# Optimization experiments

Measured on AMD Instinct MI355X. Metric: run time of the kernel, lower is better.

Reference implementation:

```python
import jax, jax.numpy as jnp
import numpy as np

D_MODEL = 2048
NUM_HEADS = 16
NUM_KV_HEADS = 4
D_HEAD = D_MODEL // NUM_HEADS  # 128
GROUPS = NUM_HEADS // NUM_KV_HEADS  # 4
ROPE_THETA = 10000.0
EPS = 1e-6


def setup_inputs() -> dict:
    key = jax.random.key(0)
    ks = jax.random.split(key, 7)
    B, S = 2, 2048
    s = 1.0 / np.sqrt(D_MODEL)
    return {
        "qkv": jax.random.normal(ks[0], (B, S, D_MODEL), dtype=jnp.float32),
        "Wq": jax.random.normal(ks[1], (D_MODEL, D_MODEL), dtype=jnp.float32) * s,
        "Wk": jax.random.normal(ks[2], (NUM_KV_HEADS * D_HEAD, D_MODEL), dtype=jnp.float32) * s,
        "Wv": jax.random.normal(ks[3], (NUM_KV_HEADS * D_HEAD, D_MODEL), dtype=jnp.float32) * s,
        "Wo": jax.random.normal(ks[4], (D_MODEL, D_MODEL), dtype=jnp.float32) * s,
        "q_gamma": jnp.ones((D_HEAD,), dtype=jnp.float32),
        "k_gamma": jnp.ones((D_HEAD,), dtype=jnp.float32),
    }


def _rmsnorm(x, gamma):
    # per-head RMSNorm over last dim (d_head)
    var = jnp.mean(jnp.square(x), axis=-1, keepdims=True)
    return x * jax.lax.rsqrt(var + EPS) * gamma


def _rope(x, cos, sin):
    # x: [B, S, H, Dh]; cos/sin: [S, Dh]
    half = x.shape[-1] // 2
    x1, x2 = x[..., :half], x[..., half:]
    rot = jnp.concatenate([-x2, x1], axis=-1)
    return x * cos[None, :, None, :] + rot * sin[None, :, None, :]


def reference(qkv, Wq, Wk, Wv, Wo, q_gamma, k_gamma):
    B, S, D = qkv.shape
    q = jnp.einsum("bsd,ed->bse", qkv, Wq).reshape(B, S, NUM_HEADS, D_HEAD)
    k = jnp.einsum("bsd,ed->bse", qkv, Wk).reshape(B, S, NUM_KV_HEADS, D_HEAD)
    v = jnp.einsum("bsd,ed->bse", qkv, Wv).reshape(B, S, NUM_KV_HEADS, D_HEAD)

    q = _rmsnorm(q, q_gamma)
    k = _rmsnorm(k, k_gamma)

    # RoPE, position_ids = arange(S)
    pos = jnp.arange(S, dtype=jnp.float32)
    inv_freq = 1.0 / (ROPE_THETA ** (jnp.arange(0, D_HEAD, 2, dtype=jnp.float32) / D_HEAD))
    ang = pos[:, None] * inv_freq[None, :]                 # [S, Dh/2]
    cos = jnp.concatenate([jnp.cos(ang), jnp.cos(ang)], axis=-1)  # [S, Dh]
    sin = jnp.concatenate([jnp.sin(ang), jnp.sin(ang)], axis=-1)
    q = _rope(q, cos, sin)
    k = _rope(k, cos, sin)

    # [B, H, S, Dh]
    q = q.transpose(0, 2, 1, 3)
    k = k.transpose(0, 2, 1, 3)
    v = v.transpose(0, 2, 1, 3)
    # GQA: repeat kv heads
    k = jnp.repeat(k, GROUPS, axis=1)
    v = jnp.repeat(v, GROUPS, axis=1)

    scale = 1.0 / np.sqrt(D_HEAD)
    scores = jnp.einsum("bhqd,bhkd->bhqk", q, k) * scale
    causal = jnp.tril(jnp.ones((S, S), dtype=bool))
    scores = jnp.where(causal[None, None], scores, jnp.finfo(scores.dtype).min)
    probs = jax.nn.softmax(scores, axis=-1)
    attended = jnp.einsum("bhqk,bhkd->bhqd", probs, v)     # [B, H, S, Dh]
    attended = attended.transpose(0, 2, 1, 3).reshape(B, S, D)
    return jnp.einsum("bsd,ed->bse", attended, Wo)
```

## Files before the change

kernel.cpp:

```cpp
#include <hip/hip_runtime.h>

#define S_LEN 2048
#define B_SZ 2
#define DMODEL 2048
#define NHEADS 16
#define NKV 4
#define DHEAD 128
#define SCALE 0.08838834764831845f
#define KVB 32

typedef __bf16 bf16x8 __attribute__((ext_vector_type(8)));
typedef __bf16 bf16x4 __attribute__((ext_vector_type(4)));
typedef float f32x4 __attribute__((ext_vector_type(4)));

#define MFMA(a, b, c) __builtin_amdgcn_mfma_f32_16x16x32_bf16(a, b, c, 0, 0, 0)

__device__ __forceinline__ void gload_lds16(const __bf16* g, __bf16* l) {
    __builtin_amdgcn_global_load_lds(
        (const __attribute__((address_space(1))) unsigned int*)g,
        (__attribute__((address_space(3))) unsigned int*)l, 16, 0, 0);
}

__global__ __launch_bounds__(256) void convert_kernel(
    const float* __restrict__ s0, const float* __restrict__ s1,
    const float* __restrict__ s2, const float* __restrict__ s3,
    const float* __restrict__ s4,
    __bf16* __restrict__ d0, __bf16* __restrict__ d1, __bf16* __restrict__ d2,
    __bf16* __restrict__ d3, __bf16* __restrict__ d4,
    float* __restrict__ cosT, float* __restrict__ sinT) {
    if (blockIdx.y == 5) {
        int i = blockIdx.x * 256 + threadIdx.x;
        int s = i >> 6, d = i & 63;
        float freq = powf(10000.0f, -(2.0f * (float)d) / 128.0f);
        float ang = (float)s * freq;
        cosT[i] = cosf(ang);
        sinT[i] = sinf(ang);
        return;
    }
    const float* s;
    __bf16* d;
    int n8;
    switch (blockIdx.y) {
        case 0: s = s0; d = d0; n8 = (B_SZ * S_LEN * DMODEL) / 8; break;
        case 1: s = s1; d = d1; n8 = (DMODEL * DMODEL) / 8; break;
        case 2: s = s2; d = d2; n8 = (NKV * DHEAD * DMODEL) / 8; break;
        case 3: s = s3; d = d3; n8 = (NKV * DHEAD * DMODEL) / 8; break;
        default: s = s4; d = d4; n8 = (DMODEL * DMODEL) / 8; break;
    }
    for (int i = blockIdx.x * 256 + threadIdx.x; i < n8; i += 512 * 256) {
        float4 a = ((const float4*)s)[2 * i];
        float4 b = ((const float4*)s)[2 * i + 1];
        bf16x8 o = {(__bf16)a.x, (__bf16)a.y, (__bf16)a.z, (__bf16)a.w,
                    (__bf16)b.x, (__bf16)b.y, (__bf16)b.z, (__bf16)b.w};
        *(bf16x8*)&d[i * 8] = o;
    }
}

template <int BM>
__device__ __forceinline__ void gemm256(const __bf16* __restrict__ A,
                                        const __bf16* __restrict__ W,
                                        int bm, int bn, int K,
                                        f32x4 (&acc)[BM / 32][4],
                                        __bf16* arena) {
    constexpr int MI = BM / 32;
    constexpr int ALT = BM / 64;
    constexpr int QM = MI / 4;
    __bf16* As = arena;
    __bf16* Bs = arena + 2 * BM * 64;
    const int tid = threadIdx.x;
    const int lane = tid & 63;
    const int wave = tid >> 6;
    const int lr = lane & 15, lk = lane >> 4;
    const int wr = wave >> 2;
    const int wc = wave & 3;
    const int sRow = lane >> 3;
    const int sCol = 8 * ((lane & 7) ^ sRow);

    auto stageA = [&](int bi, int k0) {
#pragma unroll
        for (int it = 0; it < ALT; ++it) {
            const int row = it * 64 + wave * 8 + sRow;
            gload_lds16(A + (size_t)(bm + row) * K + k0 + sCol,
                        As + bi * BM * 64 + it * 4096 + wave * 512);
        }
    };
    auto stageB = [&](int bi, int k0) {
#pragma unroll
        for (int it = 0; it < 4; ++it) {
            const int row = it * 64 + wave * 8 + sRow;
            gload_lds16(W + (size_t)(bn + row) * K + k0 + sCol,
                        Bs + bi * 16384 + it * 4096 + wave * 512);
        }
    };

#pragma unroll
    for (int mi = 0; mi < MI; ++mi)
#pragma unroll
        for (int ni = 0; ni < 4; ++ni) acc[mi][ni] = (f32x4){0.f, 0.f, 0.f, 0.f};

    const int NT = K >> 6;
    stageA(0, 0);
    stageB(0, 0);
    stageA(1, 64);
    stageB(1, 64);
    if constexpr (BM == 256) asm volatile("s_waitcnt vmcnt(8)" ::: "memory");
    else                     asm volatile("s_waitcnt vmcnt(6)" ::: "memory");
    __builtin_amdgcn_s_barrier();

    for (int t = 0; t < NT; ++t) {
        const int bi = t & 1;
        bf16x8 af[MI][2], bfr[4][2];
        auto rdA = [&](int i, int kk) {
            const int r = wr * (BM / 2) + i * 16 + lr;
            const int slot = (kk * 4 + lk) ^ (r & 7);
            af[i][kk] = *(const bf16x8*)&As[bi * BM * 64 + r * 64 + slot * 8];
        };
        auto quad = [&](int q) {
            __builtin_amdgcn_s_setprio(1);
#pragma unroll
            for (int mi = q * QM; mi < (q + 1) * QM; ++mi)
#pragma unroll
                for (int kk = 0; kk < 2; ++kk)
#pragma unroll
                    for (int ni = 0; ni < 4; ++ni)
                        acc[mi][ni] = MFMA(af[mi][kk], bfr[ni][kk], acc[mi][ni]);
            __builtin_amdgcn_s_setprio(0);
        };

#pragma unroll
        for (int i = 0; i < 4; ++i)
#pragma unroll
            for (int kk = 0; kk < 2; ++kk) {
                const int r = wc * 64 + i * 16 + lr;
                const int slot = (kk * 4 + lk) ^ (r & 7);
                bfr[i][kk] = *(const bf16x8*)&Bs[bi * 16384 + r * 64 + slot * 8];
            }
#pragma unroll
        for (int i = 0; i < QM; ++i)
#pragma unroll
            for (int kk = 0; kk < 2; ++kk) rdA(i, kk);
        __builtin_amdgcn_s_barrier();
        asm volatile("s_waitcnt lgkmcnt(0)" ::: "memory");
        __builtin_amdgcn_sched_barrier(0);
        quad(0);
        __builtin_amdgcn_s_barrier();

#pragma unroll
        for (int i = QM; i < MI; ++i)
#pragma unroll
            for (int kk = 0; kk < 2; ++kk) rdA(i, kk);
        __builtin_amdgcn_s_barrier();
        asm volatile("s_waitcnt lgkmcnt(0)" ::: "memory");
        __builtin_amdgcn_sched_barrier(0);
        quad(1);
        __builtin_amdgcn_s_barrier();

        if (t + 2 < NT) stageA(bi, (t + 2) * 64);
        quad(2);
        __builtin_amdgcn_s_barrier();

        if (t + 2 < NT) stageB(bi, (t + 2) * 64);
        quad(3);
        if (t + 1 < NT) {
            if (t + 2 < NT) {
                if constexpr (BM == 256) asm volatile("s_waitcnt vmcnt(8)" ::: "memory");
                else                     asm volatile("s_waitcnt vmcnt(6)" ::: "memory");
            } else {
                asm volatile("s_waitcnt vmcnt(0)" ::: "memory");
            }
            __builtin_amdgcn_s_barrier();
        }
    }
}

__global__ __launch_bounds__(512, 2) void qkv_proj_kernel(
    const __bf16* __restrict__ qkvb, const __bf16* __restrict__ Wq,
    const __bf16* __restrict__ Wk, const __bf16* __restrict__ Wv,
    const float* __restrict__ qg, const float* __restrict__ kg,
    const float* __restrict__ cosT, const float* __restrict__ sinT,
    __bf16* __restrict__ qb, __bf16* __restrict__ kb, __bf16* __restrict__ vt) {
    __shared__ alignas(16) __bf16 arena[4 * 256 * 64];
    const int id = (blockIdx.x & 7) * 24 + (blockIdx.x >> 3);
    const int bmi = id / 12, bni = id % 12;
    const int bm = bmi * 256;
    const __bf16* W;
    int bn;
    if (bni < 8)       { W = Wq; bn = bni * 256; }
    else if (bni < 10) { W = Wk; bn = (bni - 8) * 256; }
    else               { W = Wv; bn = (bni - 10) * 256; }

    f32x4 acc[8][4];
    gemm256<256>(qkvb, W, bm, bn, 2048, acc, arena);

    const int tid = threadIdx.x;
    const int lane = tid & 63, wave = tid >> 6;
    const int lr = lane & 15, lk = lane >> 4;
    const int wr = wave >> 2, wc = wave & 3;
    const int dc0 = (wc & 1) * 64;

    if (bni < 10) {
        const bool isQ = (bni < 8);
        const float* gamma = isQ ? qg : kg;
        const float scl = isQ ? SCALE : 1.0f;
        const int hh = (isQ ? bni * 2 : (bni - 8) * 2) + (wc >> 1);
        const int nh = isQ ? NHEADS : NKV;
        __bf16* outb = isQ ? qb : kb;
        float g[4];
#pragma unroll
        for (int ni = 0; ni < 4; ++ni) g[ni] = gamma[dc0 + ni * 16 + lr];

        float* xbuf = (float*)arena;
        float* ssbuf = (float*)((char*)arena + 70 * 1024);

        float rs[8][4];
#pragma unroll
        for (int mi = 0; mi < 8; ++mi)
#pragma unroll
            for (int r = 0; r < 4; ++r) {
                float ss = 0.f;
#pragma unroll
                for (int ni = 0; ni < 4; ++ni) ss += acc[mi][ni][r] * acc[mi][ni][r];
                ss += __shfl_xor(ss, 1);
                ss += __shfl_xor(ss, 2);
                ss += __shfl_xor(ss, 4);
                ss += __shfl_xor(ss, 8);
                if (lr == 0) ssbuf[wc * 256 + wr * 128 + mi * 16 + lk * 4 + r] = ss;
            }
        __syncthreads();
#pragma unroll
        for (int mi = 0; mi < 8; ++mi)
#pragma unroll
            for (int r = 0; r < 4; ++r) {
                const int rowl = wr * 128 + mi * 16 + lk * 4 + r;
                const float tot = ssbuf[wc * 256 + rowl] + ssbuf[(wc ^ 1) * 256 + rowl];
                rs[mi][r] = rsqrtf(tot * (1.0f / 128.0f) + 1e-6f) * scl;
            }
        __syncthreads();

#pragma unroll
        for (int ch = 0; ch < 4; ++ch) {
            float y[2][4][4];
#pragma unroll
            for (int m2 = 0; m2 < 2; ++m2)
#pragma unroll
                for (int ni = 0; ni < 4; ++ni)
#pragma unroll
                    for (int r = 0; r < 4; ++r) {
                        const int mi = ch * 2 + m2;
                        y[m2][ni][r] = acc[mi][ni][r] * rs[mi][r] * g[ni];
                        xbuf[tid * 33 + m2 * 16 + ni * 4 + r] = y[m2][ni][r];
                    }
            __syncthreads();
            float yp[2][4][4];
#pragma unroll
            for (int m2 = 0; m2 < 2; ++m2)
#pragma unroll
                for (int ni = 0; ni < 4; ++ni)
#pragma unroll
                    for (int r = 0; r < 4; ++r)
                        yp[m2][ni][r] = xbuf[(tid ^ 64) * 33 + m2 * 16 + ni * 4 + r];
#pragma unroll
            for (int m2 = 0; m2 < 2; ++m2)
#pragma unroll
                for (int r = 0; r < 4; ++r) {
                    const int mi = ch * 2 + m2;
                    const int gm = bm + wr * 128 + mi * 16 + lk * 4 + r;
                    const int bb = gm >> 11, s = gm & 2047;
                    const float* ct = cosT + s * 64;
                    const float* st = sinT + s * 64;
                    __bf16* orow = outb + (((size_t)(bb * nh + hh)) * S_LEN + s) * DHEAD;
#pragma unroll
                    for (int ni = 0; ni < 4; ++ni) {
                        const int dd = ni * 16 + lr;
                        const float c = ct[dd], sn = st[dd];
                        const float own = y[m2][ni][r], par = yp[m2][ni][r];
                        const float o = (wc & 1) ? (own * c + par * sn)
                                                 : (own * c - par * sn);
                        orow[dc0 + dd] = (__bf16)o;
                    }
                }
            __syncthreads();
        }
    } else {
        const int kvh = (bni - 10) * 2 + (wc >> 1);
#pragma unroll
        for (int mi = 0; mi < 8; ++mi) {
            const int gm = bm + wr * 128 + mi * 16 + lk * 4;
            const int bb = gm >> 11, s0 = gm & 2047;
            __bf16* vbase = vt + ((size_t)(bb * NKV + kvh)) * DHEAD * S_LEN;
#pragma unroll
            for (int ni = 0; ni < 4; ++ni) {
                const int d = dc0 + ni * 16 + lr;
                bf16x4 pk = {(__bf16)acc[mi][ni][0], (__bf16)acc[mi][ni][1],
                             (__bf16)acc[mi][ni][2], (__bf16)acc[mi][ni][3]};
                *(bf16x4*)&vbase[(size_t)d * S_LEN + s0] = pk;
            }
        }
    }
}

__global__ __launch_bounds__(512, 2) void out_proj_kernel(
    const __bf16* __restrict__ att, const __bf16* __restrict__ Wo,
    float* __restrict__ out) {
    __shared__ alignas(16) __bf16 arena[2 * 128 * 64 + 2 * 256 * 64];
    const int id = (blockIdx.x & 7) * 32 + (blockIdx.x >> 3);
    const int bm = (id >> 3) * 128, bn = (id & 7) * 256;

    f32x4 acc[4][4];
    gemm256<128>(att, Wo, bm, bn, 2048, acc, arena);

    const int lane = threadIdx.x & 63, wave = threadIdx.x >> 6;
    const int lr = lane & 15, lk = lane >> 4;
    const int wr = wave >> 2, wc = wave & 3;
#pragma unroll
    for (int mi = 0; mi < 4; ++mi)
#pragma unroll
        for (int ni = 0; ni < 4; ++ni)
#pragma unroll
            for (int r = 0; r < 4; ++r) {
                const int row = bm + wr * 64 + mi * 16 + lk * 4 + r;
                const int col = bn + wc * 64 + ni * 16 + lr;
                out[(size_t)row * DMODEL + col] = acc[mi][ni][r];
            }
}

__global__ __launch_bounds__(256, 2) void flash_kernel(
    const __bf16* __restrict__ qb, const __bf16* __restrict__ kb,
    const __bf16* __restrict__ vt, __bf16* __restrict__ att) {
    __shared__ alignas(16) __bf16 K_lds[2][32 * 128];
    __shared__ alignas(16) __bf16 V_lds[2][128 * 32];
    __shared__ alignas(16) __bf16 p_lds[4][16][40];

    const int bh = blockIdx.x;
    const int b = bh >> 4, h = bh & 15, kv = h >> 2;
    const int j = blockIdx.y;
    const int lane = threadIdx.x & 63, wave = threadIdx.x >> 6;
    const int lr = lane & 15, lk = lane >> 4;

    const int qloB = j * 64 + wave * 16;
    const int qhiB = (31 - j) * 64 + wave * 16;
    const int ntL  = ((qloB + 15) >> 5) + 1;
    const int ntHw = ((qhiB + 15) >> 5) + 1;
    const int ntH  = 64 - 2 * j;

    const __bf16* Qp = qb + ((size_t)(b * NHEADS + h)) * S_LEN * DHEAD;
    const __bf16* Kp = kb + ((size_t)(b * NKV + kv)) * S_LEN * DHEAD;
    const __bf16* Vt = vt + ((size_t)(b * NKV + kv)) * DHEAD * S_LEN;

    bf16x8 qlo[4], qhi[4];
#pragma unroll
    for (int f = 0; f < 4; ++f) {
        qlo[f] = *(const bf16x8*)&Qp[(size_t)(qloB + lr) * DHEAD + f * 32 + lk * 8];
        qhi[f] = *(const bf16x8*)&Qp[(size_t)(qhiB + lr) * DHEAD + f * 32 + lk * 8];
    }

    const int c0 = 2 * wave;
    const int l4 = lane >> 4, l15 = lane & 15;
    const int l2 = lane >> 2, l3 = lane & 3;
    const int vcol = ((l3 ^ (l2 & 3)) << 3);

    auto stage = [&](int bufi, int t) {
        const int k0s = t * KVB;
#pragma unroll
        for (int i = 0; i < 2; ++i) {
            const int c = c0 + i;
            const int rK = c * 4 + l4;
            const int kcol = ((l15 ^ (rK & 7)) << 3);
            gload_lds16(Kp + (size_t)(k0s + rK) * DHEAD + kcol, &K_lds[bufi][c * 512]);
            const int rV = c * 16 + l2;
            gload_lds16(Vt + (size_t)rV * S_LEN + k0s + vcol, &V_lds[bufi][c * 512]);
        }
    };

    f32x4 accL[8] = {}, accH[8] = {};
    float lsumL[4] = {0.f, 0.f, 0.f, 0.f}, lsumH[4] = {0.f, 0.f, 0.f, 0.f};
    const int swzK = (lr & 7) << 4;
    const int swzV = (lr & 3) << 4;

    auto frag_step = [&](const bf16x8 (&qf)[4], int qbase, f32x4 (&acc)[8],
                         float (&lsum)[4], const bf16x8 (&kf)[8],
                         const bf16x8 (&vf)[8], int k0) {
        f32x4 sc[2] = {};
        __builtin_amdgcn_s_setprio(1);
#pragma unroll
        for (int kk = 0; kk < 2; ++kk)
#pragma unroll
            for (int f = 0; f < 4; ++f)
                sc[kk] = MFMA(qf[f], kf[kk * 4 + f], sc[kk]);
        __builtin_amdgcn_s_setprio(0);
        asm volatile("s_waitcnt lgkmcnt(0)" ::: "memory");
#pragma unroll
        for (int r = 0; r < 4; ++r) {
            const int qr = qbase + lk * 4 + r;
            float s0 = sc[0][r], s1 = sc[1][r];
            if (k0 + lr > qr) s0 = -1e30f;
            if (k0 + 16 + lr > qr) s1 = -1e30f;
            float p0 = __expf(s0), p1 = __expf(s1);
            lsum[r] += p0 + p1;
            p_lds[wave][lk * 4 + r][lr] = (__bf16)p0;
            p_lds[wave][lk * 4 + r][lr + 16] = (__bf16)p1;
        }
        asm volatile("s_waitcnt lgkmcnt(0)" ::: "memory");
        bf16x8 pf = *(const bf16x8*)&p_lds[wave][lr][lk * 8];
        __builtin_amdgcn_s_setprio(1);
#pragma unroll
        for (int nf = 0; nf < 8; ++nf)
            acc[nf] = MFMA(pf, vf[nf], acc[nf]);
        __builtin_amdgcn_s_setprio(0);
    };

    int cur = 0;
    stage(0, 0);
    __syncthreads();
    for (int t = 0; t < ntH; ++t) {
        if (t + 1 < ntH) stage(cur ^ 1, t + 1);
        const int k0 = t * KVB;
        bf16x8 kf[8], vf[8];
#pragma unroll
        for (int kk = 0; kk < 2; ++kk)
#pragma unroll
            for (int f = 0; f < 4; ++f) {
                const int cb = (f * 64 + lk * 16) ^ swzK;
                kf[kk * 4 + f] =
                    *(const bf16x8*)((const char*)&K_lds[cur][(kk * 16 + lr) * 128] + cb);
            }
#pragma unroll
        for (int nf = 0; nf < 8; ++nf) {
            const int cb = (lk * 16) ^ swzV;
            vf[nf] = *(const bf16x8*)((const char*)&V_lds[cur][(nf * 16 + lr) * 32] + cb);
        }
        if (t < ntHw) frag_step(qhi, qhiB, accH, lsumH, kf, vf, k0);
        if (t < ntL)  frag_step(qlo, qloB, accL, lsumL, kf, vf, k0);
        __syncthreads();
        cur ^= 1;
    }

#pragma unroll
    for (int r = 0; r < 4; ++r) {
#pragma unroll
        for (int m = 1; m < 16; m <<= 1) {
            lsumL[r] += __shfl_xor(lsumL[r], m);
            lsumH[r] += __shfl_xor(lsumH[r], m);
        }
    }
#pragma unroll
    for (int nf = 0; nf < 8; ++nf)
#pragma unroll
        for (int r = 0; r < 4; ++r) {
            int qrL = qloB + lk * 4 + r;
            int qrH = qhiB + lk * 4 + r;
            att[((size_t)(b * S_LEN) + qrL) * DMODEL + h * DHEAD + nf * 16 + lr] =
                (__bf16)(accL[nf][r] / lsumL[r]);
            att[((size_t)(b * S_LEN) + qrH) * DMODEL + h * DHEAD + nf * 16 + lr] =
                (__bf16)(accH[nf][r] / lsumH[r]);
        }
}

extern "C" void kernel_launch(void* const* d_in, const int* in_sizes, int n_in,
                              void* d_out, int out_size, void* d_ws, size_t ws_size,
                              hipStream_t stream) {
    const float* qkv = (const float*)d_in[0];
    const float* Wq  = (const float*)d_in[1];
    const float* Wk  = (const float*)d_in[2];
    const float* Wv  = (const float*)d_in[3];
    const float* Wo  = (const float*)d_in[4];
    const float* qg  = (const float*)d_in[5];
    const float* kg  = (const float*)d_in[6];
    float* out = (float*)d_out;

    size_t off = 0;
    char* wsb = (char*)d_ws;
    auto alloc = [&](size_t n) {
        char* p = wsb + off;
        off += (n + 255) & ~(size_t)255;
        return (void*)p;
    };
    const size_t M = (size_t)B_SZ * S_LEN;
    float* cosT   = (float*)alloc((size_t)S_LEN * 64 * 4);
    float* sinT   = (float*)alloc((size_t)S_LEN * 64 * 4);
    __bf16* qb    = (__bf16*)alloc((size_t)B_SZ * NHEADS * S_LEN * DHEAD * 2);
    __bf16* kb    = (__bf16*)alloc((size_t)B_SZ * NKV * S_LEN * DHEAD * 2);
    __bf16* vt    = (__bf16*)alloc((size_t)B_SZ * NKV * DHEAD * S_LEN * 2);
    __bf16* att   = (__bf16*)alloc(M * DMODEL * 2);
    __bf16* qkv_b = (__bf16*)alloc(M * DMODEL * 2);
    __bf16* wq_b  = (__bf16*)alloc((size_t)DMODEL * DMODEL * 2);
    __bf16* wk_b  = (__bf16*)alloc((size_t)NKV * DHEAD * DMODEL * 2);
    __bf16* wv_b  = (__bf16*)alloc((size_t)NKV * DHEAD * DMODEL * 2);
    __bf16* wo_b  = (__bf16*)alloc((size_t)DMODEL * DMODEL * 2);

    convert_kernel<<<dim3(512, 6), 256, 0, stream>>>(qkv, Wq, Wk, Wv, Wo,
                                                     qkv_b, wq_b, wk_b, wv_b, wo_b,
                                                     cosT, sinT);
    qkv_proj_kernel<<<192, 512, 0, stream>>>(qkv_b, wq_b, wk_b, wv_b,
                                             qg, kg, cosT, sinT, qb, kb, vt);
    flash_kernel<<<dim3(B_SZ * NHEADS, 16), 256, 0, stream>>>(qb, kb, vt, att);
    out_proj_kernel<<<256, 512, 0, stream>>>(att, wo_b, out);
}
```

Baseline: 185.7 us.

## Use eight-phase interleaved load/MFMA schedule for QKV projection GEMM

Adds a new 256x256 GEMM mainloop that splits each K-tile into four compute phases, each reading its own A/B fragments from LDS and issuing half-tile global-to-LDS loads staggered across phases. The QKV projection kernel now uses this schedule instead of the generic gemm256<256>, aiming to spread memory traffic more evenly and overlap it better with MFMA work. The generic path's waitcnt is simplified to the BM=128 value, since only that instantiation remains in use. The finer-grained phases add more barriers per tile and carry risk if the vmcnt counts are wrong.

After: 187.8 us. No clear change (+1.1%).

```diff
diff --git a/kernel.cpp b/kernel.cpp
--- a/kernel.cpp
+++ b/kernel.cpp
@@ -53,6 +53,107 @@
         bf16x8 o = {(__bf16)a.x, (__bf16)a.y, (__bf16)a.z, (__bf16)a.w,
                     (__bf16)b.x, (__bf16)b.y, (__bf16)b.z, (__bf16)b.w};
         *(bf16x8*)&d[i * 8] = o;
+    }
+}
+
+__device__ __forceinline__ void gemm256_8ph(const __bf16* __restrict__ A,
+                                            const __bf16* __restrict__ W,
+                                            int bm, int bn, int K,
+                                            f32x4 (&acc)[8][4],
+                                            __bf16* arena) {
+    __bf16* As = arena;
+    __bf16* Bs = arena + 2 * 256 * 64;
+    const int tid = threadIdx.x;
+    const int lane = tid & 63;
+    const int wave = tid >> 6;
+    const int lr = lane & 15, lk = lane >> 4;
+    const int wr = wave >> 2, wc = wave & 3;
+    const int sRow = lane >> 3;
+    const int sCol = 8 * ((lane & 7) ^ sRow);
+
+    auto stageA = [&](int b, int T, int p) {
+#pragma unroll
+        for (int h = 0; h < 2; ++h) {
+            const int it = h * 2 + p;
+            const int row = it * 64 + wave * 8 + sRow;
+            gload_lds16(A + (size_t)(bm + row) * K + T * 64 + sCol,
+                        As + b * 16384 + it * 4096 + wave * 512);
+        }
+    };
+    auto stageB = [&](int b, int T, int p) {
+#pragma unroll
+        for (int i = 0; i < 2; ++i) {
+            const int m = i * 8 + wave;
+            const int blk = m >> 2;
+            const int row = blk * 64 + p * 32 + (m & 3) * 8 + sRow;
+            gload_lds16(W + (size_t)(bn + row) * K + T * 64 + sCol,
+                        Bs + b * 16384 + blk * 4096 + p * 2048 + (m & 3) * 512);
+        }
+    };
+
+#pragma unroll
+    for (int mi = 0; mi < 8; ++mi)
+#pragma unroll
+        for (int ni = 0; ni < 4; ++ni) acc[mi][ni] = (f32x4){0.f, 0.f, 0.f, 0.f};
+
+    const int NT = K >> 6;
+    stageA(0, 0, 0);
+    stageB(0, 0, 0);
+    stageA(0, 0, 1);
+    stageB(0, 0, 1);
+    stageA(1, 1, 0);
+    stageB(1, 1, 0);
+    asm volatile("s_waitcnt vmcnt(8)" ::: "memory");
+    __builtin_amdgcn_s_barrier();
+
+    for (int t = 0; t < NT; ++t) {
+        const int bi = t & 1;
+#pragma unroll
+        for (int q = 0; q < 4; ++q) {
+            const int mi0 = (q >> 1) * 4, ni0 = (q & 1) * 2;
+            bf16x8 af[4][2], bfr[2][2];
+#pragma unroll
+            for (int i = 0; i < 4; ++i)
+#pragma unroll
+                for (int kk = 0; kk < 2; ++kk) {
+                    const int r = wr * 128 + (mi0 + i) * 16 + lr;
+                    const int slot = (kk * 4 + lk) ^ (r & 7);
+                    af[i][kk] = *(const bf16x8*)&As[bi * 16384 + r * 64 + slot * 8];
+                }
+#pragma unroll
+            for (int j = 0; j < 2; ++j)
+#pragma unroll
+                for (int kk = 0; kk < 2; ++kk) {
+                    const int r = wc * 64 + (ni0 + j) * 16 + lr;
+                    const int slot = (kk * 4 + lk) ^ (r & 7);
+                    bfr[j][kk] = *(const bf16x8*)&Bs[bi * 16384 + r * 64 + slot * 8];
+                }
+            if (q == 0)      { if (t + 1 < NT) stageA(bi ^ 1, t + 1, 1); }
+            else if (q == 1) { if (t + 1 < NT) stageB(bi ^ 1, t + 1, 1); }
+            else if (q == 2) { if (t + 2 < NT) stageA(bi, t + 2, 0); }
+            else             { if (t + 2 < NT) stageB(bi, t + 2, 0); }
+
+            asm volatile("s_waitcnt lgkmcnt(0)" ::: "memory");
+            __builtin_amdgcn_sched_barrier(0);
+            __builtin_amdgcn_s_setprio(1);
+#pragma unroll
+            for (int i = 0; i < 4; ++i)
+#pragma unroll
+                for (int j = 0; j < 2; ++j)
+#pragma unroll
+                    for (int kk = 0; kk < 2; ++kk)
+                        acc[mi0 + i][ni0 + j] =
+                            MFMA(af[i][kk], bfr[j][kk], acc[mi0 + i][ni0 + j]);
+            __builtin_amdgcn_s_setprio(0);
+            if (q == 0) {
+                if (t == NT - 1) asm volatile("s_waitcnt vmcnt(0)" ::: "memory");
+                else             asm volatile("s_waitcnt vmcnt(6)" ::: "memory");
+            } else if (q == 3 && t + 1 < NT) {
+                if (t + 1 == NT - 1) asm volatile("s_waitcnt vmcnt(4)" ::: "memory");
+                else                 asm volatile("s_waitcnt vmcnt(8)" ::: "memory");
+            }
+            __builtin_amdgcn_s_barrier();
+        }
     }
 }
 
@@ -103,8 +204,7 @@
     stageB(0, 0);
     stageA(1, 64);
     stageB(1, 64);
-    if constexpr (BM == 256) asm volatile("s_waitcnt vmcnt(8)" ::: "memory");
-    else                     asm volatile("s_waitcnt vmcnt(6)" ::: "memory");
+    asm volatile("s_waitcnt vmcnt(6)" ::: "memory");
     __builtin_amdgcn_s_barrier();
 
     for (int t = 0; t < NT; ++t) {
@@ -162,12 +262,8 @@
         if (t + 2 < NT) stageB(bi, (t + 2) * 64);
         quad(3);
         if (t + 1 < NT) {
-            if (t + 2 < NT) {
-                if constexpr (BM == 256) asm volatile("s_waitcnt vmcnt(8)" ::: "memory");
-                else                     asm volatile("s_waitcnt vmcnt(6)" ::: "memory");
-            } else {
-                asm volatile("s_waitcnt vmcnt(0)" ::: "memory");
-            }
+            if (t + 2 < NT) asm volatile("s_waitcnt vmcnt(6)" ::: "memory");
+            else            asm volatile("s_waitcnt vmcnt(0)" ::: "memory");
             __builtin_amdgcn_s_barrier();
         }
     }
@@ -190,7 +286,7 @@
     else               { W = Wv; bn = (bni - 10) * 256; }
 
     f32x4 acc[8][4];
-    gemm256<256>(qkvb, W, bm, bn, 2048, acc, arena);
+    gemm256_8ph(qkvb, W, bm, bn, 2048, acc, arena);
 
     const int tid = threadIdx.x;
     const int lane = tid & 63, wave = tid >> 6;
```
